# Optimization experiments

Measured on AMD Instinct MI355X. Metric: run time of the kernel, lower is better.

Reference implementation:

```python
import jax, jax.numpy as jnp
import numpy as np

B = 131072
SEQ = 64
HID = 20
LSTM_W_BITS = 8
LSTM_A_BITS = 6
LIN_W_BITS = 8
LIN_A_BITS = 6
IO_BITS = 8


def _ste(x, q):
    # straight-through estimator: forward value q, gradient of identity
    return x + jax.lax.stop_gradient(q - x)


def fq_signed_dyn(x, bits):
    # symmetric per-tensor fake quant, dynamic max-abs scale
    qmax = 2.0 ** (bits - 1) - 1.0
    s = jnp.maximum(jnp.max(jnp.abs(x)), 1e-8) / qmax
    q = jnp.clip(jnp.round(x / s), -qmax, qmax) * s
    return _ste(x, q)


def fq_unsigned_dyn(x, bits):
    # unsigned per-tensor fake quant (for post-ReLU activations)
    qmax = 2.0 ** bits - 1.0
    s = jnp.maximum(jnp.max(x), 1e-8) / qmax
    q = jnp.clip(jnp.round(x / s), 0.0, qmax) * s
    return _ste(x, q)


def fq_sigmoid(x, bits):
    # quantized sigmoid: output in [0,1], fixed scale 1/(2^b-1)
    qmax = 2.0 ** bits - 1.0
    y = jax.nn.sigmoid(x)
    return _ste(y, jnp.round(y * qmax) / qmax)


def fq_tanh(x, bits):
    # quantized tanh: output in [-1,1], fixed scale 1/(2^(b-1)-1)
    qmax = 2.0 ** (bits - 1) - 1.0
    y = jnp.tanh(x)
    return _ste(y, jnp.round(y * qmax) / qmax)


def setup_inputs() -> dict:
    key = jax.random.key(0)
    ks = jax.random.split(key, 10)

    def u(k, shape, fan_in):
        lim = 1.0 / np.sqrt(fan_in)
        return jax.random.uniform(k, shape, jnp.float32, -lim, lim)

    x = jax.random.normal(ks[0], (B, SEQ), jnp.float32)
    w_ih = u(ks[1], (4 * HID, 1), HID)      # LSTM input weights (input_size=1)
    w_hh = u(ks[2], (4 * HID, HID), HID)    # LSTM recurrent weights
    b = u(ks[3], (4 * HID,), HID)           # combined bias (bias_quant=None)
    W1 = u(ks[4], (64, HID), HID)
    b1 = u(ks[5], (64,), HID)
    W2 = u(ks[6], (32, 64), 64)
    b2 = u(ks[7], (32,), 64)
    W3 = u(ks[8], (4, 32), 32)
    b3 = u(ks[9], (4,), 32)
    return dict(x=x, w_ih=w_ih, w_hh=w_hh, b=b, W1=W1, b1=b1, W2=W2, b2=b2, W3=W3, b3=b3)


def reference(x, w_ih, w_hh, b, W1, b1, W2, b2, W3, b3):
    # io_quant (Int8ActPerTensorFloat) on LSTM input
    xq = fq_signed_dyn(x, IO_BITS)
    w_ih_q = fq_signed_dyn(w_ih, LSTM_W_BITS)
    w_hh_q = fq_signed_dyn(w_hh, LSTM_W_BITS)

    xs = xq.reshape(B, SEQ, 1).transpose(1, 0, 2)  # (SEQ, B, 1)

    def step(carry, x_t):
        h, c = carry
        gates = x_t @ w_ih_q.T + h @ w_hh_q.T + b   # (B, 4*HID)
        gates = fq_signed_dyn(gates, LSTM_A_BITS)   # gate_acc quant
        i_g, f_g, g_g, o_g = jnp.split(gates, 4, axis=-1)
        i = fq_sigmoid(i_g, LSTM_A_BITS)
        f = fq_sigmoid(f_g, LSTM_A_BITS)
        g = fq_tanh(g_g, LSTM_A_BITS)
        o = fq_sigmoid(o_g, LSTM_A_BITS)
        c_new = fq_signed_dyn(f * c + i * g, LSTM_A_BITS)  # cell_state quant
        h_new = o * fq_tanh(c_new, LSTM_A_BITS)
        return (h_new, c_new), None

    h0 = jnp.zeros((B, HID), jnp.float32)
    (h_last, _), _ = jax.lax.scan(step, (h0, h0), xs)

    # quantized MLP head: QuantReLU -> QuantLinear x3 -> ReLU
    out = fq_unsigned_dyn(jax.nn.relu(h_last), LIN_A_BITS)
    out = out @ fq_signed_dyn(W1, LIN_W_BITS).T + b1
    out = fq_unsigned_dyn(jax.nn.relu(out), LIN_A_BITS)
    out = out @ fq_signed_dyn(W2, LIN_W_BITS).T + b2
    out = fq_unsigned_dyn(jax.nn.relu(out), LIN_A_BITS)
    out = out @ fq_signed_dyn(W3, LIN_W_BITS).T + b3
    return jax.nn.relu(out)
```

## Files before the change

kernel.cpp:

```cpp
#include <hip/hip_runtime.h>
#include <math.h>


#define NBLK  256
#define NTHR  512
#define SEQL  64
#define HIDN  20
#define G4    80

__device__ __forceinline__ float tanh_xla(float x){
  const float kClamp = 7.90531110763549805f;
  float xc = fminf(fmaxf(x, -kClamp), kClamp);
  float x2 = xc*xc;
  float p = fmaf(x2, -2.76076847742355e-16f, 2.00018790482477e-13f);
  p = fmaf(x2, p, -8.60467152213735e-11f);
  p = fmaf(x2, p,  5.12229709037114e-08f);
  p = fmaf(x2, p,  1.48572235717979e-05f);
  p = fmaf(x2, p,  6.37261928875436e-04f);
  p = fmaf(x2, p,  4.89352455891786e-03f);
  p = p * xc;
  float q = fmaf(x2, 1.19825839466702e-06f, 1.18534705686654e-04f);
  q = fmaf(x2, q, 2.26843463243900e-03f);
  q = fmaf(x2, q, 4.89352518554385e-03f);
  float y = p / q;
  return (fabsf(x) < 4e-4f) ? x : y;
}

__device__ __forceinline__ float qround(float x, float s, float inv_s, float tol){
  float n = rintf(__fmul_rn(x, inv_s));
  float e = fmaf(-n, s, x);
  if (__builtin_expect(fabsf(fabsf(e) - 0.5f*s) <= tol*s, 0))
    n = rintf(x / s);
  return n;
}

__device__ __forceinline__ float phase_max(float lmax, int phase,
                                           unsigned long long* slots,
                                           int blk, int tid, float* s_red, float* s_bc)
{
  #pragma unroll
  for (int off=32; off; off>>=1) lmax = fmaxf(lmax, __shfl_xor(lmax, off, 64));
  int wid = tid>>6, lane = tid&63;
  if (lane==0) s_red[wid] = lmax;
  __syncthreads();
  if (wid==0) {
    float bm = s_red[lane&7];
    bm = fmaxf(bm, __shfl_xor(bm,4,64));
    bm = fmaxf(bm, __shfl_xor(bm,2,64));
    bm = fmaxf(bm, __shfl_xor(bm,1,64));
    unsigned long long* sp = slots + (size_t)(phase&1)*NBLK;
    const unsigned long long tagw = ((unsigned long long)(unsigned)(phase+1))<<32;
    if (lane==0)
      __hip_atomic_store(sp+blk, tagw | (unsigned long long)__float_as_uint(bm),
                         __ATOMIC_RELAXED, __HIP_MEMORY_SCOPE_AGENT);
    unsigned long long v0,v1,v2,v3;
    const unsigned int tag = (unsigned int)(phase+1);
    for (;;) {
      v0 = __hip_atomic_load(sp+lane,     __ATOMIC_RELAXED, __HIP_MEMORY_SCOPE_AGENT);
      v1 = __hip_atomic_load(sp+lane+64,  __ATOMIC_RELAXED, __HIP_MEMORY_SCOPE_AGENT);
      v2 = __hip_atomic_load(sp+lane+128, __ATOMIC_RELAXED, __HIP_MEMORY_SCOPE_AGENT);
      v3 = __hip_atomic_load(sp+lane+192, __ATOMIC_RELAXED, __HIP_MEMORY_SCOPE_AGENT);
      bool ok = ((unsigned)(v0>>32)==tag) && ((unsigned)(v1>>32)==tag) &&
                ((unsigned)(v2>>32)==tag) && ((unsigned)(v3>>32)==tag);
      if (__all(ok)) break;
      __builtin_amdgcn_s_sleep(1);
    }
    unsigned int m0 = (unsigned int)v0, m1 = (unsigned int)v1;
    unsigned int m2 = (unsigned int)v2, m3 = (unsigned int)v3;
    unsigned int m = m0>m1?m0:m1; if (m2>m) m=m2; if (m3>m) m=m3;
    #pragma unroll
    for (int off=32; off; off>>=1) {
      unsigned int o = (unsigned int)__shfl_xor((int)m, off, 64);
      if (o>m) m=o;
    }
    if (lane==0) *s_bc = __uint_as_float(m);
  }
  __syncthreads();
  return *s_bc;
}

__global__ void kinit(float* __restrict__ ws) {
  int i = threadIdx.x;
  for (; i < 1152; i += 256) ws[i] = 0.0f;
}

__global__ void kmaxabs_x(const float4* __restrict__ x4, int n4, int* __restrict__ xmax_bits) {
  float m = 0.f;
  int stride = gridDim.x*blockDim.x;
  for (int i = blockIdx.x*blockDim.x + threadIdx.x; i < n4; i += stride) {
    float4 v = x4[i];
    m = fmaxf(fmaxf(fabsf(v.x),fabsf(v.y)), fmaxf(fmaxf(fabsf(v.z),fabsf(v.w)), m));
  }
  #pragma unroll
  for (int off=32; off; off>>=1) m = fmaxf(m, __shfl_xor(m, off, 64));
  __shared__ float red[4];
  int wid = threadIdx.x>>6, lane = threadIdx.x&63;
  if (lane==0) red[wid]=m;
  __syncthreads();
  if (threadIdx.x==0) {
    float bm = fmaxf(fmaxf(red[0],red[1]), fmaxf(red[2],red[3]));
    atomicMax(xmax_bits, __float_as_int(bm));
  }
}

__global__ void kscales(const float* __restrict__ wih, const float* __restrict__ whh,
                        const float* __restrict__ W1, const float* __restrict__ W2,
                        const float* __restrict__ W3, float* __restrict__ ws)
{
  int wid = threadIdx.x>>6, lane = threadIdx.x&63;
  const float* p; int n;
  if      (wid==0){p=wih;n=80;}   else if (wid==1){p=whh;n=1600;}
  else if (wid==2){p=W1;n=1280;}  else if (wid==3){p=W2;n=2048;}
  else            {p=W3;n=128;}
  float m=0.f;
  for (int i=lane;i<n;i+=64) m=fmaxf(m,fabsf(p[i]));
  #pragma unroll
  for (int off=32; off; off>>=1) m=fmaxf(m,__shfl_xor(m,off,64));
  if (lane==0) ws[9+wid]=fmaxf(m,1e-8f)/127.0f;
  if (threadIdx.x==0) {
    float xm = __int_as_float(((const int*)ws)[0]);
    ws[8]=fmaxf(xm,1e-8f)/127.0f;
  }
}

__global__ void __launch_bounds__(NTHR, 2)
kmain(const float* __restrict__ x, const float* __restrict__ w_ih,
      const float* __restrict__ w_hh, const float* __restrict__ bias,
      const float* __restrict__ W1, const float* __restrict__ b1,
      const float* __restrict__ W2, const float* __restrict__ b2,
      const float* __restrict__ W3, const float* __restrict__ b3,
      float* __restrict__ out, float* __restrict__ ws)
{
  __shared__ float s_whh[HIDN*G4];
  __shared__ float s_wih[G4];
  __shared__ float s_b[G4];
  __shared__ float s_W1[HIDN*64];
  __shared__ float s_b1v[64];
  __shared__ float s_W2[64*32];
  __shared__ float s_b2v[32];
  __shared__ float s_W3[32*4];
  __shared__ float s_b3v[4];
  __shared__ float s_lutsig[63];
  __shared__ float s_luttg[63];
  __shared__ float s_luttc[63];
  __shared__ float s_red[8];
  __shared__ float s_bc;

  const int tid = threadIdx.x;
  const int blk = blockIdx.x;
  unsigned long long* slots = (unsigned long long*)(ws + 64);

  const float sx   = ws[8];
  const float swih = ws[9];
  const float swhh = ws[10];
  const float sw1  = ws[11];
  const float sw2  = ws[12];
  const float sw3  = ws[13];

  for (int i = tid; i < G4; i += NTHR) {
    s_wih[i] = fminf(fmaxf(rintf(w_ih[i]/swih), -127.f), 127.f)*swih;
    s_b[i]   = bias[i];
  }
  for (int i = tid; i < HIDN*G4; i += NTHR) {
    int j = i/HIDN, k = i - j*HIDN;
    s_whh[k*G4+j] = fminf(fmaxf(rintf(w_hh[i]/swhh), -127.f), 127.f)*swhh;
  }
  for (int i = tid; i < 64*HIDN; i += NTHR) {
    int j = i/HIDN, k = i - j*HIDN;
    s_W1[k*64+j] = fminf(fmaxf(rintf(W1[i]/sw1), -127.f), 127.f)*sw1;
  }
  for (int i = tid; i < 32*64; i += NTHR) {
    int j = i>>6, k = i&63;
    s_W2[k*32+j] = fminf(fmaxf(rintf(W2[i]/sw2), -127.f), 127.f)*sw2;
  }
  for (int i = tid; i < 4*32; i += NTHR) {
    int j = i>>5, k = i&31;
    s_W3[k*4+j] = fminf(fmaxf(rintf(W3[i]/sw3), -127.f), 127.f)*sw3;
  }
  if (tid < 64) s_b1v[tid] = b1[tid];
  if (tid < 32) s_b2v[tid] = b2[tid];
  if (tid < 4)  s_b3v[tid] = b3[tid];
  __syncthreads();

  const long bI = (long)blk*NTHR + tid;
  const float* xrow = x + bI*SEQL;
  const float inv_sx = __builtin_amdgcn_rcpf(sx);

  float h[HIDN], c[HIDN];
  #pragma unroll
  for (int k=0;k<HIDN;++k){ h[k]=0.f; c[k]=0.f; }

  float4 x4v;
  #pragma unroll 1
  for (int t=0; t<SEQL; ++t) {
    if ((t&3)==0) x4v = *(const float4*)(xrow + t);
    float xv = (t&3)==1 ? x4v.y : ((t&3)==2 ? x4v.z : ((t&3)==3 ? x4v.w : x4v.x));
    float xq = __fmul_rn(fminf(fmaxf(qround(xv, sx, inv_sx, 1e-4f), -127.f), 127.f), sx);

    float hw[G4];
    #pragma unroll
    for (int j=0;j<G4;++j) hw[j]=0.f;
    #pragma unroll
    for (int k=0;k<HIDN;++k) {
      float hk = h[k];
      #pragma unroll
      for (int j=0;j<G4;j+=4) {
        float4 w = *(const float4*)&s_whh[k*G4+j];
        hw[j]   = fmaf(hk, w.x, hw[j]);
        hw[j+1] = fmaf(hk, w.y, hw[j+1]);
        hw[j+2] = fmaf(hk, w.z, hw[j+2]);
        hw[j+3] = fmaf(hk, w.w, hw[j+3]);
      }
    }
    float lm = 0.f;
    #pragma unroll
    for (int j=0;j<G4;++j) {
      float g = __fadd_rn(__fadd_rn(__fmul_rn(xq, s_wih[j]), hw[j]), s_b[j]);
      hw[j] = g;
      lm = fmaxf(lm, fabsf(g));
    }
    float gm = phase_max(lm, 2*t, slots, blk, tid, s_red, &s_bc);
    float s1 = fmaxf(gm, 1e-8f)/31.0f;
    float inv1 = __builtin_amdgcn_rcpf(s1);

    if (tid < 63) {
      float q  = __fmul_rn((float)(tid-31), s1);
      float ti = tanh_xla(0.5f*q);
      int ni = (int)rintf(fmaf(0.5f, ti, 0.5f)*63.0f);
      ni = min(max(ni,0),63);
      s_lutsig[tid] = (float)ni/63.0f;
    } else if (tid >= 64 && tid < 127) {
      int n = tid - 64 - 31;
      float q  = __fmul_rn((float)n, s1);
      float tg = tanh_xla(q);
      int ng = (int)rintf(tg*31.0f);
      ng = min(max(ng,-31),31);
      s_luttg[tid-64] = (float)ng/31.0f;
    }
    __syncthreads();

    float og[HIDN];
    float lm2 = 0.f;
    #pragma unroll
    for (int k=0;k<HIDN;++k) {
      int ii = min(max((int)qround(hw[k   ], s1, inv1, 2e-5f),-31),31)+31;
      int fi = min(max((int)qround(hw[20+k], s1, inv1, 2e-5f),-31),31)+31;
      int gi = min(max((int)qround(hw[40+k], s1, inv1, 2e-5f),-31),31)+31;
      int oi = min(max((int)qround(hw[60+k], s1, inv1, 2e-5f),-31),31)+31;
      float iv = s_lutsig[ii];
      float fv = s_lutsig[fi];
      float gv = s_luttg[gi];
      og[k]    = s_lutsig[oi];
      float pc = __fadd_rn(__fmul_rn(fv, c[k]), __fmul_rn(iv, gv));
      c[k] = pc;
      lm2 = fmaxf(lm2, fabsf(pc));
    }
    float gm2 = phase_max(lm2, 2*t+1, slots, blk, tid, s_red, &s_bc);
    float s2 = fmaxf(gm2, 1e-8f)/31.0f;
    float inv2 = __builtin_amdgcn_rcpf(s2);
    if (tid < 63) {
      float q  = __fmul_rn((float)(tid-31), s2);
      float tc = tanh_xla(q);
      int nc = (int)rintf(tc*31.0f);
      nc = min(max(nc,-31),31);
      s_luttc[tid] = (float)nc/31.0f;
    }
    __syncthreads();
    #pragma unroll
    for (int k=0;k<HIDN;++k) {
      int m = min(max((int)qround(c[k], s2, inv2, 2e-5f),-31),31);
      float cn = __fmul_rn((float)m, s2);
      c[k] = cn;
      h[k] = __fmul_rn(og[k], s_luttc[m+31]);
    }
  }

  float lm3 = 0.f;
  float a0[HIDN];
  #pragma unroll
  for (int k=0;k<HIDN;++k){ float r = fmaxf(h[k],0.f); a0[k]=r; lm3=fmaxf(lm3,r); }
  float gm3 = phase_max(lm3, 128, slots, blk, tid, s_red, &s_bc);
  float s3 = fmaxf(gm3,1e-8f)/63.0f;
  float inv3 = __builtin_amdgcn_rcpf(s3);
  #pragma unroll
  for (int k=0;k<HIDN;++k)
    a0[k] = __fmul_rn(fminf(fmaxf(qround(a0[k], s3, inv3, 4e-5f),0.f),63.f), s3);

  float o1[64];
  #pragma unroll
  for (int j=0;j<64;++j) o1[j] = 0.f;
  #pragma unroll
  for (int k=0;k<HIDN;++k) {
    float ak = a0[k];
    #pragma unroll
    for (int j=0;j<64;j+=4) {
      float4 w = *(const float4*)&s_W1[k*64+j];
      o1[j]   = fmaf(ak,w.x,o1[j]);
      o1[j+1] = fmaf(ak,w.y,o1[j+1]);
      o1[j+2] = fmaf(ak,w.z,o1[j+2]);
      o1[j+3] = fmaf(ak,w.w,o1[j+3]);
    }
  }
  float lm4 = 0.f;
  #pragma unroll
  for (int j=0;j<64;++j){ o1[j]=fmaxf(__fadd_rn(o1[j],s_b1v[j]),0.f); lm4=fmaxf(lm4,o1[j]); }
  float gm4 = phase_max(lm4, 129, slots, blk, tid, s_red, &s_bc);
  float s4 = fmaxf(gm4,1e-8f)/63.0f;
  float inv4 = __builtin_amdgcn_rcpf(s4);
  #pragma unroll
  for (int j=0;j<64;++j)
    o1[j] = __fmul_rn(fminf(fmaxf(qround(o1[j], s4, inv4, 4e-5f),0.f),63.f), s4);

  float o2[32];
  #pragma unroll
  for (int j=0;j<32;++j) o2[j] = 0.f;
  #pragma unroll
  for (int k=0;k<64;++k) {
    float ak = o1[k];
    #pragma unroll
    for (int j=0;j<32;j+=4) {
      float4 w = *(const float4*)&s_W2[k*32+j];
      o2[j]   = fmaf(ak,w.x,o2[j]);
      o2[j+1] = fmaf(ak,w.y,o2[j+1]);
      o2[j+2] = fmaf(ak,w.z,o2[j+2]);
      o2[j+3] = fmaf(ak,w.w,o2[j+3]);
    }
  }
  float lm5=0.f;
  #pragma unroll
  for (int j=0;j<32;++j){ o2[j]=fmaxf(__fadd_rn(o2[j],s_b2v[j]),0.f); lm5=fmaxf(lm5,o2[j]); }
  float gm5 = phase_max(lm5, 130, slots, blk, tid, s_red, &s_bc);
  float s5 = fmaxf(gm5,1e-8f)/63.0f;
  float inv5 = __builtin_amdgcn_rcpf(s5);
  #pragma unroll
  for (int j=0;j<32;++j)
    o2[j] = __fmul_rn(fminf(fmaxf(qround(o2[j], s5, inv5, 4e-5f),0.f),63.f), s5);

  float o3[4] = {0.f,0.f,0.f,0.f};
  #pragma unroll
  for (int k=0;k<32;++k) {
    float ak = o2[k];
    float4 w = *(const float4*)&s_W3[k*4];
    o3[0]=fmaf(ak,w.x,o3[0]); o3[1]=fmaf(ak,w.y,o3[1]);
    o3[2]=fmaf(ak,w.z,o3[2]); o3[3]=fmaf(ak,w.w,o3[3]);
  }
  float4 res;
  res.x = fmaxf(__fadd_rn(o3[0],s_b3v[0]),0.f);
  res.y = fmaxf(__fadd_rn(o3[1],s_b3v[1]),0.f);
  res.z = fmaxf(__fadd_rn(o3[2],s_b3v[2]),0.f);
  res.w = fmaxf(__fadd_rn(o3[3],s_b3v[3]),0.f);
  ((float4*)out)[bI] = res;
}

extern "C" void kernel_launch(void* const* d_in, const int* in_sizes, int n_in,
                              void* d_out, int out_size, void* d_ws, size_t ws_size,
                              hipStream_t stream) {
  const float* x    = (const float*)d_in[0];
  const float* w_ih = (const float*)d_in[1];
  const float* w_hh = (const float*)d_in[2];
  const float* b    = (const float*)d_in[3];
  const float* W1   = (const float*)d_in[4];
  const float* b1   = (const float*)d_in[5];
  const float* W2   = (const float*)d_in[6];
  const float* b2   = (const float*)d_in[7];
  const float* W3   = (const float*)d_in[8];
  const float* b3   = (const float*)d_in[9];
  float* out = (float*)d_out;
  float* ws  = (float*)d_ws;

  int n4 = in_sizes[0]/4;
  kinit<<<1,256,0,stream>>>(ws);
  kmaxabs_x<<<1024,256,0,stream>>>((const float4*)x, n4, (int*)ws);
  kscales<<<1,320,0,stream>>>(w_ih,w_hh,W1,W2,W3,ws);
  kmain<<<dim3(NBLK), dim3(NTHR), 0, stream>>>(x,w_ih,w_hh,b,W1,b1,W2,b2,W3,b3,out,ws);
}
```

Baseline: 1.343 ms.

## Pre-quantize weights in prep kernel and read them via uniform global loads

Weight quantization and transposition move from every kmain block into a single prep kernel that writes quantized weights to workspace. kmain drops its LDS weight copies and reads weights and biases directly from global memory with thread-uniform addresses. The compiler can then use scalar loads and constant cache instead of LDS reads. This removes redundant per-block prologue work and LDS traffic. The risk is scalar-cache pressure or SGPR spills in the unrolled 80-wide recurrent loop.

```diff
diff --git a/kernel.cpp b/kernel.cpp
--- a/kernel.cpp
+++ b/kernel.cpp
@@ -7,6 +7,13 @@
 #define SEQL  64
 #define HIDN  20
 #define G4    80
+
+#define OF_WIH 0
+#define OF_WHH 80
+#define OF_W1  1680
+#define OF_W2  2960
+#define OF_W3  5008
+#define NQ     5136
 
 __device__ __forceinline__ float tanh_xla(float x){
   const float kClamp = 7.90531110763549805f;
@@ -81,7 +88,7 @@
 
 __global__ void kinit(float* __restrict__ ws) {
   int i = threadIdx.x;
-  for (; i < 1152; i += 256) ws[i] = 0.0f;
+  for (; i < 1088; i += 256) ws[i] = 0.0f;
 }
 
 __global__ void kmaxabs_x(const float4* __restrict__ x4, int n4, int* __restrict__ xmax_bits) {
@@ -103,43 +110,49 @@
   }
 }
 
-__global__ void kscales(const float* __restrict__ wih, const float* __restrict__ whh,
-                        const float* __restrict__ W1, const float* __restrict__ W2,
-                        const float* __restrict__ W3, float* __restrict__ ws)
+__global__ void kprep(const float* __restrict__ wih, const float* __restrict__ whh,
+                      const float* __restrict__ W1, const float* __restrict__ W2,
+                      const float* __restrict__ W3, float* __restrict__ ws)
 {
-  int wid = threadIdx.x>>6, lane = threadIdx.x&63;
-  const float* p; int n;
-  if      (wid==0){p=wih;n=80;}   else if (wid==1){p=whh;n=1600;}
-  else if (wid==2){p=W1;n=1280;}  else if (wid==3){p=W2;n=2048;}
-  else            {p=W3;n=128;}
-  float m=0.f;
-  for (int i=lane;i<n;i+=64) m=fmaxf(m,fabsf(p[i]));
-  #pragma unroll
-  for (int off=32; off; off>>=1) m=fmaxf(m,__shfl_xor(m,off,64));
-  if (lane==0) ws[9+wid]=fmaxf(m,1e-8f)/127.0f;
-  if (threadIdx.x==0) {
+  __shared__ float sc[6];
+  int tid = threadIdx.x, wid = tid>>6, lane = tid&63;
+  if (wid < 5) {
+    const float* p; int n;
+    if      (wid==0){p=wih;n=80;}   else if (wid==1){p=whh;n=1600;}
+    else if (wid==2){p=W1;n=1280;}  else if (wid==3){p=W2;n=2048;}
+    else            {p=W3;n=128;}
+    float m=0.f;
+    for (int i=lane;i<n;i+=64) m=fmaxf(m,fabsf(p[i]));
+    #pragma unroll
+    for (int off=32; off; off>>=1) m=fmaxf(m,__shfl_xor(m,off,64));
+    if (lane==0) sc[1+wid]=fmaxf(m,1e-8f)/127.0f;
+  }
+  if (tid==0) {
     float xm = __int_as_float(((const int*)ws)[0]);
-    ws[8]=fmaxf(xm,1e-8f)/127.0f;
+    float sx = fmaxf(xm,1e-8f)/127.0f;
+    sc[0] = sx; ws[8] = sx;
+  }
+  __syncthreads();
+  float* wq = ws + 1088;
+  for (int i=tid; i<NQ; i+=512) {
+    float s, v; int dst;
+    if (i < 80)        { s=sc[1]; v=wih[i]; dst=OF_WIH + i; }
+    else if (i < 1680) { int e=i-80;   int j=e/20, k=e-j*20; s=sc[2]; v=whh[e]; dst=OF_WHH + k*80 + j; }
+    else if (i < 2960) { int e=i-1680; int j=e/20, k=e-j*20; s=sc[3]; v=W1[e];  dst=OF_W1  + k*64 + j; }
+    else if (i < 5008) { int e=i-2960; int j=e>>6, k=e&63;   s=sc[4]; v=W2[e];  dst=OF_W2  + k*32 + j; }
+    else               { int e=i-5008; int j=e>>5, k=e&31;   s=sc[5]; v=W3[e];  dst=OF_W3  + k*4  + j; }
+    wq[dst] = fminf(fmaxf(rintf(v/s), -127.f), 127.f)*s;
   }
 }
 
 __global__ void __launch_bounds__(NTHR, 2)
-kmain(const float* __restrict__ x, const float* __restrict__ w_ih,
-      const float* __restrict__ w_hh, const float* __restrict__ bias,
-      const float* __restrict__ W1, const float* __restrict__ b1,
-      const float* __restrict__ W2, const float* __restrict__ b2,
-      const float* __restrict__ W3, const float* __restrict__ b3,
-      float* __restrict__ out, float* __restrict__ ws)
+kmain(const float* __restrict__ x, const float* __restrict__ bias,
+      const float* __restrict__ b1, const float* __restrict__ b2,
+      const float* __restrict__ b3, float* __restrict__ out,
+      unsigned long long* __restrict__ slots,
+      const float* __restrict__ wq,
+      const float* __restrict__ wsbase)
 {
-  __shared__ float s_whh[HIDN*G4];
-  __shared__ float s_wih[G4];
-  __shared__ float s_b[G4];
-  __shared__ float s_W1[HIDN*64];
-  __shared__ float s_b1v[64];
-  __shared__ float s_W2[64*32];
-  __shared__ float s_b2v[32];
-  __shared__ float s_W3[32*4];
-  __shared__ float s_b3v[4];
   __shared__ float s_lutsig[63];
   __shared__ float s_luttg[63];
   __shared__ float s_luttc[63];
@@ -148,39 +161,10 @@
 
   const int tid = threadIdx.x;
   const int blk = blockIdx.x;
-  unsigned long long* slots = (unsigned long long*)(ws + 64);
-
-  const float sx   = ws[8];
-  const float swih = ws[9];
-  const float swhh = ws[10];
-  const float sw1  = ws[11];
-  const float sw2  = ws[12];
-  const float sw3  = ws[13];
-
-  for (int i = tid; i < G4; i += NTHR) {
-    s_wih[i] = fminf(fmaxf(rintf(w_ih[i]/swih), -127.f), 127.f)*swih;
-    s_b[i]   = bias[i];
-  }
-  for (int i = tid; i < HIDN*G4; i += NTHR) {
-    int j = i/HIDN, k = i - j*HIDN;
-    s_whh[k*G4+j] = fminf(fmaxf(rintf(w_hh[i]/swhh), -127.f), 127.f)*swhh;
-  }
-  for (int i = tid; i < 64*HIDN; i += NTHR) {
-    int j = i/HIDN, k = i - j*HIDN;
-    s_W1[k*64+j] = fminf(fmaxf(rintf(W1[i]/sw1), -127.f), 127.f)*sw1;
-  }
-  for (int i = tid; i < 32*64; i += NTHR) {
-    int j = i>>6, k = i&63;
-    s_W2[k*32+j] = fminf(fmaxf(rintf(W2[i]/sw2), -127.f), 127.f)*sw2;
-  }
-  for (int i = tid; i < 4*32; i += NTHR) {
-    int j = i>>5, k = i&31;
-    s_W3[k*4+j] = fminf(fmaxf(rintf(W3[i]/sw3), -127.f), 127.f)*sw3;
-  }
-  if (tid < 64) s_b1v[tid] = b1[tid];
-  if (tid < 32) s_b2v[tid] = b2[tid];
-  if (tid < 4)  s_b3v[tid] = b3[tid];
-  __syncthreads();
+
+  const float sx = wsbase[8];
+  const float* wih = wq + OF_WIH;
+  const float* whh = wq + OF_WHH;
 
   const long bI = (long)blk*NTHR + tid;
   const float* xrow = x + bI*SEQL;
@@ -204,18 +188,13 @@
     for (int k=0;k<HIDN;++k) {
       float hk = h[k];
       #pragma unroll
-      for (int j=0;j<G4;j+=4) {
-        float4 w = *(const float4*)&s_whh[k*G4+j];
-        hw[j]   = fmaf(hk, w.x, hw[j]);
-        hw[j+1] = fmaf(hk, w.y, hw[j+1]);
-        hw[j+2] = fmaf(hk, w.z, hw[j+2]);
-        hw[j+3] = fmaf(hk, w.w, hw[j+3]);
-      }
+      for (int j=0;j<G4;++j)
+        hw[j] = fmaf(hk, whh[k*G4+j], hw[j]);
     }
     float lm = 0.f;
     #pragma unroll
     for (int j=0;j<G4;++j) {
-      float g = __fadd_rn(__fadd_rn(__fmul_rn(xq, s_wih[j]), hw[j]), s_b[j]);
+      float g = __fadd_rn(__fadd_rn(__fmul_rn(xq, wih[j]), hw[j]), bias[j]);
       hw[j] = g;
       lm = fmaxf(lm, fabsf(g));
     }
@@ -275,6 +254,10 @@
     }
   }
 
+  const float* W1q = wq + OF_W1;
+  const float* W2q = wq + OF_W2;
+  const float* W3q = wq + OF_W3;
+
   float lm3 = 0.f;
   float a0[HIDN];
   #pragma unroll
@@ -293,17 +276,11 @@
   for (int k=0;k<HIDN;++k) {
     float ak = a0[k];
     #pragma unroll
-    for (int j=0;j<64;j+=4) {
-      float4 w = *(const float4*)&s_W1[k*64+j];
-      o1[j]   = fmaf(ak,w.x,o1[j]);
-      o1[j+1] = fmaf(ak,w.y,o1[j+1]);
-      o1[j+2] = fmaf(ak,w.z,o1[j+2]);
-      o1[j+3] = fmaf(ak,w.w,o1[j+3]);
-    }
+    for (int j=0;j<64;++j) o1[j] = fmaf(ak, W1q[k*64+j], o1[j]);
   }
   float lm4 = 0.f;
   #pragma unroll
-  for (int j=0;j<64;++j){ o1[j]=fmaxf(__fadd_rn(o1[j],s_b1v[j]),0.f); lm4=fmaxf(lm4,o1[j]); }
+  for (int j=0;j<64;++j){ o1[j]=fmaxf(__fadd_rn(o1[j],b1[j]),0.f); lm4=fmaxf(lm4,o1[j]); }
   float gm4 = phase_max(lm4, 129, slots, blk, tid, s_red, &s_bc);
   float s4 = fmaxf(gm4,1e-8f)/63.0f;
   float inv4 = __builtin_amdgcn_rcpf(s4);
@@ -318,17 +295,11 @@
   for (int k=0;k<64;++k) {
     float ak = o1[k];
     #pragma unroll
-    for (int j=0;j<32;j+=4) {
-      float4 w = *(const float4*)&s_W2[k*32+j];
-      o2[j]   = fmaf(ak,w.x,o2[j]);
-      o2[j+1] = fmaf(ak,w.y,o2[j+1]);
-      o2[j+2] = fmaf(ak,w.z,o2[j+2]);
-      o2[j+3] = fmaf(ak,w.w,o2[j+3]);
-    }
+    for (int j=0;j<32;++j) o2[j] = fmaf(ak, W2q[k*32+j], o2[j]);
   }
   float lm5=0.f;
   #pragma unroll
-  for (int j=0;j<32;++j){ o2[j]=fmaxf(__fadd_rn(o2[j],s_b2v[j]),0.f); lm5=fmaxf(lm5,o2[j]); }
+  for (int j=0;j<32;++j){ o2[j]=fmaxf(__fadd_rn(o2[j],b2[j]),0.f); lm5=fmaxf(lm5,o2[j]); }
   float gm5 = phase_max(lm5, 130, slots, blk, tid, s_red, &s_bc);
   float s5 = fmaxf(gm5,1e-8f)/63.0f;
   float inv5 = __builtin_amdgcn_rcpf(s5);
@@ -340,15 +311,14 @@
   #pragma unroll
   for (int k=0;k<32;++k) {
     float ak = o2[k];
-    float4 w = *(const float4*)&s_W3[k*4];
-    o3[0]=fmaf(ak,w.x,o3[0]); o3[1]=fmaf(ak,w.y,o3[1]);
-    o3[2]=fmaf(ak,w.z,o3[2]); o3[3]=fmaf(ak,w.w,o3[3]);
+    #pragma unroll
+    for (int j=0;j<4;++j) o3[j] = fmaf(ak, W3q[k*4+j], o3[j]);
   }
   float4 res;
-  res.x = fmaxf(__fadd_rn(o3[0],s_b3v[0]),0.f);
-  res.y = fmaxf(__fadd_rn(o3[1],s_b3v[1]),0.f);
-  res.z = fmaxf(__fadd_rn(o3[2],s_b3v[2]),0.f);
-  res.w = fmaxf(__fadd_rn(o3[3],s_b3v[3]),0.f);
+  res.x = fmaxf(__fadd_rn(o3[0],b3[0]),0.f);
+  res.y = fmaxf(__fadd_rn(o3[1],b3[1]),0.f);
+  res.z = fmaxf(__fadd_rn(o3[2],b3[2]),0.f);
+  res.w = fmaxf(__fadd_rn(o3[3],b3[3]),0.f);
   ((float4*)out)[bI] = res;
 }
 
@@ -371,6 +341,8 @@
   int n4 = in_sizes[0]/4;
   kinit<<<1,256,0,stream>>>(ws);
   kmaxabs_x<<<1024,256,0,stream>>>((const float4*)x, n4, (int*)ws);
-  kscales<<<1,320,0,stream>>>(w_ih,w_hh,W1,W2,W3,ws);
-  kmain<<<dim3(NBLK), dim3(NTHR), 0, stream>>>(x,w_ih,w_hh,b,W1,b1,W2,b2,W3,b3,out,ws);
-}
+  kprep<<<1,512,0,stream>>>(w_ih,w_hh,W1,W2,W3,ws);
+  kmain<<<dim3(NBLK), dim3(NTHR), 0, stream>>>(
+      x, b, b1, b2, b3, out,
+      (unsigned long long*)(ws + 64), ws + 1088, ws);
+}
```

Result: slower. 1.879 ms (+39.9%).

## Replace block barriers in grid max with tagged LDS spin flags and packed FMA

Applied to the files above, without the earlier changes.

The per-step grid-wide max reduction no longer uses __syncthreads inside phase_max. Waves now publish tagged 64-bit values into LDS and spin on them, and all threads spin-read a tagged broadcast slot instead of meeting at a barrier. The recurrent matvec is also rewritten with two-wide vector FMA, which can map to packed fp32 FMA. The gate bias and input-weight loads are vectorised to float4. The aim is to cut barrier cost and ALU issue in the latency-bound scan, at the cost of LDS spin-polling by waiting waves and reliance on volatile LDS ordering being correct.

```diff
diff --git a/kernel.cpp b/kernel.cpp
--- a/kernel.cpp
+++ b/kernel.cpp
@@ -7,6 +7,9 @@
 #define SEQL  64
 #define HIDN  20
 #define G4    80
+
+typedef float f2 __attribute__((ext_vector_type(2)));
+typedef unsigned long long u64;
 
 __device__ __forceinline__ float tanh_xla(float x){
   const float kClamp = 7.90531110763549805f;
@@ -35,33 +38,35 @@
 }
 
 __device__ __forceinline__ float phase_max(float lmax, int phase,
-                                           unsigned long long* slots,
-                                           int blk, int tid, float* s_red, float* s_bc)
+                                           u64* slots, int blk, int tid,
+                                           volatile u64* s_red64,
+                                           volatile u64* s_bc64)
 {
   #pragma unroll
   for (int off=32; off; off>>=1) lmax = fmaxf(lmax, __shfl_xor(lmax, off, 64));
-  int wid = tid>>6, lane = tid&63;
-  if (lane==0) s_red[wid] = lmax;
-  __syncthreads();
+  const int wid = tid>>6, lane = tid&63;
+  const unsigned int tag = (unsigned int)(phase+1);
+  const u64 tw = ((u64)tag)<<32;
+  if (lane==0) s_red64[wid] = tw | (u64)__float_as_uint(lmax);
   if (wid==0) {
-    float bm = s_red[lane&7];
+    u64 pv = 0;
+    if (lane<8) { do { pv = s_red64[lane]; } while ((unsigned int)(pv>>32)!=tag); }
+    float bm = (lane<8) ? __uint_as_float((unsigned int)pv) : 0.f;
     bm = fmaxf(bm, __shfl_xor(bm,4,64));
     bm = fmaxf(bm, __shfl_xor(bm,2,64));
     bm = fmaxf(bm, __shfl_xor(bm,1,64));
-    unsigned long long* sp = slots + (size_t)(phase&1)*NBLK;
-    const unsigned long long tagw = ((unsigned long long)(unsigned)(phase+1))<<32;
+    u64* sp = slots + (size_t)(phase&1)*NBLK;
     if (lane==0)
-      __hip_atomic_store(sp+blk, tagw | (unsigned long long)__float_as_uint(bm),
+      __hip_atomic_store(sp+blk, tw | (u64)__float_as_uint(bm),
                          __ATOMIC_RELAXED, __HIP_MEMORY_SCOPE_AGENT);
-    unsigned long long v0,v1,v2,v3;
-    const unsigned int tag = (unsigned int)(phase+1);
+    u64 v0,v1,v2,v3;
     for (;;) {
       v0 = __hip_atomic_load(sp+lane,     __ATOMIC_RELAXED, __HIP_MEMORY_SCOPE_AGENT);
       v1 = __hip_atomic_load(sp+lane+64,  __ATOMIC_RELAXED, __HIP_MEMORY_SCOPE_AGENT);
       v2 = __hip_atomic_load(sp+lane+128, __ATOMIC_RELAXED, __HIP_MEMORY_SCOPE_AGENT);
       v3 = __hip_atomic_load(sp+lane+192, __ATOMIC_RELAXED, __HIP_MEMORY_SCOPE_AGENT);
-      bool ok = ((unsigned)(v0>>32)==tag) && ((unsigned)(v1>>32)==tag) &&
-                ((unsigned)(v2>>32)==tag) && ((unsigned)(v3>>32)==tag);
+      bool ok = ((unsigned int)(v0>>32)==tag) && ((unsigned int)(v1>>32)==tag) &&
+                ((unsigned int)(v2>>32)==tag) && ((unsigned int)(v3>>32)==tag);
       if (__all(ok)) break;
       __builtin_amdgcn_s_sleep(1);
     }
@@ -73,10 +78,11 @@
       unsigned int o = (unsigned int)__shfl_xor((int)m, off, 64);
       if (o>m) m=o;
     }
-    if (lane==0) *s_bc = __uint_as_float(m);
-  }
-  __syncthreads();
-  return *s_bc;
+    if (lane==0) *s_bc64 = tw | (u64)m;
+  }
+  u64 bv;
+  do { bv = *s_bc64; } while ((unsigned int)(bv>>32)!=tag);
+  return __uint_as_float((unsigned int)bv);
 }
 
 __global__ void kinit(float* __restrict__ ws) {
@@ -143,12 +149,12 @@
   __shared__ float s_lutsig[63];
   __shared__ float s_luttg[63];
   __shared__ float s_luttc[63];
-  __shared__ float s_red[8];
-  __shared__ float s_bc;
+  __shared__ u64 s_red64[8];
+  __shared__ u64 s_bc64;
 
   const int tid = threadIdx.x;
   const int blk = blockIdx.x;
-  unsigned long long* slots = (unsigned long long*)(ws + 64);
+  u64* slots = (u64*)(ws + 64);
 
   const float sx   = ws[8];
   const float swih = ws[9];
@@ -197,29 +203,37 @@
     float xv = (t&3)==1 ? x4v.y : ((t&3)==2 ? x4v.z : ((t&3)==3 ? x4v.w : x4v.x));
     float xq = __fmul_rn(fminf(fmaxf(qround(xv, sx, inv_sx, 1e-4f), -127.f), 127.f), sx);
 
-    float hw[G4];
-    #pragma unroll
-    for (int j=0;j<G4;++j) hw[j]=0.f;
+    f2 hw2[40];
+    #pragma unroll
+    for (int j=0;j<40;++j) { hw2[j].x = 0.f; hw2[j].y = 0.f; }
     #pragma unroll
     for (int k=0;k<HIDN;++k) {
       float hk = h[k];
+      f2 hk2; hk2.x = hk; hk2.y = hk;
+      const float4* w4 = (const float4*)&s_whh[k*G4];
       #pragma unroll
-      for (int j=0;j<G4;j+=4) {
-        float4 w = *(const float4*)&s_whh[k*G4+j];
-        hw[j]   = fmaf(hk, w.x, hw[j]);
-        hw[j+1] = fmaf(hk, w.y, hw[j+1]);
-        hw[j+2] = fmaf(hk, w.z, hw[j+2]);
-        hw[j+3] = fmaf(hk, w.w, hw[j+3]);
+      for (int j4=0;j4<20;++j4) {
+        float4 w = w4[j4];
+        f2 wlo; wlo.x = w.x; wlo.y = w.y;
+        f2 whi; whi.x = w.z; whi.y = w.w;
+        hw2[2*j4]   = __builtin_elementwise_fma(hk2, wlo, hw2[2*j4]);
+        hw2[2*j4+1] = __builtin_elementwise_fma(hk2, whi, hw2[2*j4+1]);
       }
     }
+    float* hw = (float*)hw2;
     float lm = 0.f;
     #pragma unroll
-    for (int j=0;j<G4;++j) {
-      float g = __fadd_rn(__fadd_rn(__fmul_rn(xq, s_wih[j]), hw[j]), s_b[j]);
-      hw[j] = g;
-      lm = fmaxf(lm, fabsf(g));
-    }
-    float gm = phase_max(lm, 2*t, slots, blk, tid, s_red, &s_bc);
+    for (int j4=0;j4<20;++j4) {
+      float4 wi = *(const float4*)&s_wih[j4*4];
+      float4 bb = *(const float4*)&s_b[j4*4];
+      float g0 = __fadd_rn(__fadd_rn(__fmul_rn(xq, wi.x), hw[j4*4  ]), bb.x);
+      float g1 = __fadd_rn(__fadd_rn(__fmul_rn(xq, wi.y), hw[j4*4+1]), bb.y);
+      float g2 = __fadd_rn(__fadd_rn(__fmul_rn(xq, wi.z), hw[j4*4+2]), bb.z);
+      float g3 = __fadd_rn(__fadd_rn(__fmul_rn(xq, wi.w), hw[j4*4+3]), bb.w);
+      hw[j4*4  ]=g0; hw[j4*4+1]=g1; hw[j4*4+2]=g2; hw[j4*4+3]=g3;
+      lm = fmaxf(lm, fmaxf(fmaxf(fabsf(g0),fabsf(g1)), fmaxf(fabsf(g2),fabsf(g3))));
+    }
+    float gm = phase_max(lm, 2*t, slots, blk, tid, s_red64, &s_bc64);
     float s1 = fmaxf(gm, 1e-8f)/31.0f;
     float inv1 = __builtin_amdgcn_rcpf(s1);
 
@@ -255,7 +269,7 @@
       c[k] = pc;
       lm2 = fmaxf(lm2, fabsf(pc));
     }
-    float gm2 = phase_max(lm2, 2*t+1, slots, blk, tid, s_red, &s_bc);
+    float gm2 = phase_max(lm2, 2*t+1, slots, blk, tid, s_red64, &s_bc64);
     float s2 = fmaxf(gm2, 1e-8f)/31.0f;
     float inv2 = __builtin_amdgcn_rcpf(s2);
     if (tid < 63) {
@@ -279,7 +293,7 @@
   float a0[HIDN];
   #pragma unroll
   for (int k=0;k<HIDN;++k){ float r = fmaxf(h[k],0.f); a0[k]=r; lm3=fmaxf(lm3,r); }
-  float gm3 = phase_max(lm3, 128, slots, blk, tid, s_red, &s_bc);
+  float gm3 = phase_max(lm3, 128, slots, blk, tid, s_red64, &s_bc64);
   float s3 = fmaxf(gm3,1e-8f)/63.0f;
   float inv3 = __builtin_amdgcn_rcpf(s3);
   #pragma unroll
@@ -304,7 +318,7 @@
   float lm4 = 0.f;
   #pragma unroll
   for (int j=0;j<64;++j){ o1[j]=fmaxf(__fadd_rn(o1[j],s_b1v[j]),0.f); lm4=fmaxf(lm4,o1[j]); }
-  float gm4 = phase_max(lm4, 129, slots, blk, tid, s_red, &s_bc);
+  float gm4 = phase_max(lm4, 129, slots, blk, tid, s_red64, &s_bc64);
   float s4 = fmaxf(gm4,1e-8f)/63.0f;
   float inv4 = __builtin_amdgcn_rcpf(s4);
   #pragma unroll
@@ -329,7 +343,7 @@
   float lm5=0.f;
   #pragma unroll
   for (int j=0;j<32;++j){ o2[j]=fmaxf(__fadd_rn(o2[j],s_b2v[j]),0.f); lm5=fmaxf(lm5,o2[j]); }
-  float gm5 = phase_max(lm5, 130, slots, blk, tid, s_red, &s_bc);
+  float gm5 = phase_max(lm5, 130, slots, blk, tid, s_red64, &s_bc64);
   float s5 = fmaxf(gm5,1e-8f)/63.0f;
   float inv5 = __builtin_amdgcn_rcpf(s5);
   #pragma unroll
```

Measured after the change: 1.326 ms. About the same (-1.3%).
